# Performance work log

Hardware: AMD Instinct MI355X
Metric: run time of the kernel (lower is better)

Reference implementation:

```python
import jax, jax.numpy as jnp
import numpy as np

N_NODES = 100000
N_EDGES = 1000000
IN_DIM = 128
OUT_DIM = 64
NEG_SLOPE = 0.2


def setup_inputs() -> dict:
    key = jax.random.key(0)
    k = jax.random.split(key, 6)
    h = jax.random.normal(k[0], (N_NODES, IN_DIM), dtype=jnp.float32)
    # xavier-uniform-ish scales for linear weights
    W_w = jax.random.uniform(k[1], (OUT_DIM, IN_DIM), dtype=jnp.float32,
                             minval=-1.0, maxval=1.0) * np.sqrt(6.0 / (IN_DIM + OUT_DIM))
    W_b = jnp.zeros((OUT_DIM,), dtype=jnp.float32)
    a_w = jax.random.uniform(k[2], (1, 2 * OUT_DIM), dtype=jnp.float32,
                             minval=-1.0, maxval=1.0) * np.sqrt(6.0 / (2 * OUT_DIM + 1))
    a_b = jnp.zeros((1,), dtype=jnp.float32)
    edge_index = jax.random.randint(k[3], (2, N_EDGES), 0, N_NODES, dtype=jnp.int64)
    return {"h": h, "W_w": W_w, "W_b": W_b, "a_w": a_w, "a_b": a_b,
            "edge_index": edge_index}


def reference(h, W_w, W_b, a_w, a_b, edge_index):
    # Wh = W(h): [N, D_out]
    Wh = h @ W_w.T + W_b
    src, tgt = edge_index[0], edge_index[1]
    D = Wh.shape[1]
    # a([e_src, e_tgt]) decomposes: score = Wh@a_src per-node + Wh@a_tgt per-node,
    # gathered by edge (avoids materializing the [E, 2D] concat).
    s_src = Wh @ a_w[0, :D]   # [N]
    s_tgt = Wh @ a_w[0, D:]   # [N]
    logits = jax.nn.leaky_relu(s_src[src] + s_tgt[tgt] + a_b[0], NEG_SLOPE)  # [E]
    # NOTE: global softmax over all edges (dim=0), faithful to the source.
    attn = jax.nn.softmax(logits, axis=0)
    e_src = Wh[src]  # [E, D] gather
    messages = jnp.zeros_like(Wh).at[tgt].add(attn[:, None] * e_src)  # scatter-add
    return jax.nn.leaky_relu(messages, NEG_SLOPE)
```

## Files before the change

### kernel.cpp

```cpp
#include <hip/hip_runtime.h>
#include <math.h>

#define N_NODES 100000
#define N_EDGES 1000000
#define IN_DIM  128
#define OUT_DIM 64
#define NEG     0.2f

#define SCAN_BLOCKS 391
#define EDGE_BLOCKS 3907
#define GEMM_BLOCKS 782
#define FUSED_BLOCKS (GEMM_BLOCKS + EDGE_BLOCKS)

typedef __attribute__((ext_vector_type(8))) short short8;
typedef __attribute__((ext_vector_type(4))) float f32x4;

#define MFMA(A, B, C) __builtin_amdgcn_mfma_f32_16x16x32_bf16(A, B, C, 0, 0, 0)

union U16 { unsigned u[4]; short8 s; };

__device__ __forceinline__ void split8(const float* x, short8& hi, short8& lo) {
    U16 H, L;
#pragma unroll
    for (int i = 0; i < 4; ++i) {
        float a = x[2 * i], b = x[2 * i + 1];
        unsigned ua = __float_as_uint(a), ub = __float_as_uint(b);
        unsigned ha = ua & 0xffff0000u, hb = ub & 0xffff0000u;
        H.u[i] = (ua >> 16) | hb;
        float la = a - __uint_as_float(ha);
        float lb = b - __uint_as_float(hb);
        L.u[i] = (__float_as_uint(la) >> 16) | (__float_as_uint(lb) & 0xffff0000u);
    }
    hi = H.s; lo = L.s;
}

__global__ __launch_bounds__(256, 4) void kA_fused(
    const float* __restrict__ h, const float* __restrict__ W,
    const float* __restrict__ Wb, const float* __restrict__ aw,
    float* __restrict__ Wh, float* __restrict__ s_src, float* __restrict__ s_tgt,
    const int* __restrict__ ei, unsigned* __restrict__ deg8,
    unsigned* __restrict__ rank)
{
    __shared__ float4 smem4[2176];

    if ((blockIdx.x % 6) != 0) {
        const int hid = blockIdx.x - blockIdx.x / 6 - 1;
        const int e = hid * 256 + threadIdx.x;
        if (e < N_EDGES) {
            int t = ei[N_EDGES + e];
            rank[e] = atomicAdd(&deg8[(size_t)(hid & 7) * N_NODES + t], 1u);
        }
        return;
    }

    unsigned short* wfh = (unsigned short*)smem4;
    unsigned short* wfl = wfh + 8192;

    const int tid  = threadIdx.x;
    const int lane = tid & 63, w = tid >> 6;
    const int c = lane & 15, g = lane >> 4;
    const int n0 = (blockIdx.x / 6) * 128;

#pragma unroll
    for (int it = 0; it < 4; ++it) {
        int U = tid + 256 * it;
        int pos = U >> 6, l = U & 63;
        int nb = pos >> 2, ks = pos & 3;
        int r  = 16 * nb + (l & 15);
        int k0 = 32 * ks + 8 * (l >> 4);
        float a[8];
        *(float4*)&a[0] = *(const float4*)(W + r * IN_DIM + k0);
        *(float4*)&a[4] = *(const float4*)(W + r * IN_DIM + k0 + 4);
        short8 hi, lo; split8(a, hi, lo);
        *(short8*)(wfh + (size_t)U * 8) = hi;
        *(short8*)(wfl + (size_t)U * 8) = lo;
    }
    __syncthreads();

    const int na0 = n0 + 32 * w + c;
    const float* hp0 = h + (size_t)min(na0, N_NODES - 1) * IN_DIM + 8 * g;
    const float* hp1 = h + (size_t)min(na0 + 16, N_NODES - 1) * IN_DIM + 8 * g;

    f32x4 acc[2][4];
    {
        f32x4 z = {0.f, 0.f, 0.f, 0.f};
#pragma unroll
        for (int m = 0; m < 2; ++m)
#pragma unroll
            for (int nb = 0; nb < 4; ++nb) acc[m][nb] = z;
    }

#pragma unroll 2
    for (int ks = 0; ks < 4; ++ks) {
        short8 bh[4], bl[4];
#pragma unroll
        for (int nb = 0; nb < 4; ++nb) {
            int u = ((nb * 4 + ks) * 64 + lane) * 8;
            bh[nb] = *(const short8*)(wfh + u);
            bl[nb] = *(const short8*)(wfl + u);
        }
        float am[8];
        short8 ah, al;
        *(float4*)&am[0] = *(const float4*)(hp0 + 32 * ks);
        *(float4*)&am[4] = *(const float4*)(hp0 + 32 * ks + 4);
        split8(am, ah, al);
#pragma unroll
        for (int nb = 0; nb < 4; ++nb) {
            acc[0][nb] = MFMA(ah, bh[nb], acc[0][nb]);
            acc[0][nb] = MFMA(ah, bl[nb], acc[0][nb]);
            acc[0][nb] = MFMA(al, bh[nb], acc[0][nb]);
        }
        *(float4*)&am[0] = *(const float4*)(hp1 + 32 * ks);
        *(float4*)&am[4] = *(const float4*)(hp1 + 32 * ks + 4);
        split8(am, ah, al);
#pragma unroll
        for (int nb = 0; nb < 4; ++nb) {
            acc[1][nb] = MFMA(ah, bh[nb], acc[1][nb]);
            acc[1][nb] = MFMA(ah, bl[nb], acc[1][nb]);
            acc[1][nb] = MFMA(al, bh[nb], acc[1][nb]);
        }
    }

    float wb[4], w1[4], w2[4];
#pragma unroll
    for (int nb = 0; nb < 4; ++nb) {
        wb[nb] = Wb[16 * nb + c];
        w1[nb] = aw[16 * nb + c];
        w2[nb] = aw[OUT_DIM + 16 * nb + c];
    }
#pragma unroll
    for (int m = 0; m < 2; ++m)
#pragma unroll
        for (int r = 0; r < 4; ++r) {
            float s1 = 0.f, s2 = 0.f;
#pragma unroll
            for (int nb = 0; nb < 4; ++nb) {
                float v = acc[m][nb][r] + wb[nb];
                acc[m][nb][r] = v;
                s1 = fmaf(v, w1[nb], s1);
                s2 = fmaf(v, w2[nb], s2);
            }
#pragma unroll
            for (int mk = 1; mk < 16; mk <<= 1) {
                s1 += __shfl_xor(s1, mk);
                s2 += __shfl_xor(s2, mk);
            }
            if (c == 0) {
                int node = n0 + 32 * w + 16 * m + 4 * g + r;
                if (node < N_NODES) { s_src[node] = s1; s_tgt[node] = s2; }
            }
        }

    __syncthreads();
    float* tr = (float*)smem4;
#pragma unroll
    for (int m = 0; m < 2; ++m)
#pragma unroll
        for (int nb = 0; nb < 4; ++nb)
#pragma unroll
            for (int r = 0; r < 4; ++r)
                tr[(32 * w + 16 * m + 4 * g + r) * 68 + 16 * nb + c] = acc[m][nb][r];
    __syncthreads();

#pragma unroll
    for (int j = 0; j < 8; ++j) {
        int idx = tid + 256 * j;
        int nloc = idx >> 4, d4 = idx & 15;
        int node = n0 + nloc;
        if (node < N_NODES)
            ((float4*)Wh)[(size_t)node * 16 + d4] =
                *(const float4*)&tr[nloc * 68 + d4 * 4];
    }
}

__global__ __launch_bounds__(256) void k_mid(
    const int* __restrict__ ei, const float* __restrict__ s_src,
    const float* __restrict__ s_tgt, const float* __restrict__ ab,
    const unsigned* __restrict__ deg8,
    float* __restrict__ exv, float* __restrict__ bsum,
    unsigned* __restrict__ psum)
{
    const float ab0 = ab[0];
    float lsum = 0.f;
    const int e = blockIdx.x * 256 + threadIdx.x;
    if (e < N_EDGES) {
        int s = ei[e], t = ei[N_EDGES + e];
        float x = s_src[s] + s_tgt[t] + ab0;
        float l = x > 0.f ? x : NEG * x;
        float ex = __expf(l);
        exv[e] = ex;
        lsum = ex;
    }
#pragma unroll
    for (int off = 32; off; off >>= 1) lsum += __shfl_xor(lsum, off);
    __shared__ float ssum[4];
    if ((threadIdx.x & 63) == 0) ssum[threadIdx.x >> 6] = lsum;
    __syncthreads();
    if (threadIdx.x == 0)
        bsum[blockIdx.x] = ssum[0] + ssum[1] + ssum[2] + ssum[3];

    if (blockIdx.x < SCAN_BLOCKS) {
        const int i = blockIdx.x * 256 + threadIdx.x;
        unsigned v = 0;
        if (i < N_NODES) {
#pragma unroll
            for (int x = 0; x < 8; ++x) v += deg8[(size_t)x * N_NODES + i];
        }
#pragma unroll
        for (int off = 32; off; off >>= 1) v += __shfl_xor(v, off);
        __shared__ unsigned us[4];
        if ((threadIdx.x & 63) == 0) us[threadIdx.x >> 6] = v;
        __syncthreads();
        if (threadIdx.x == 0)
            psum[blockIdx.x] = us[0] + us[1] + us[2] + us[3];
    }
}

__global__ __launch_bounds__(512) void k_scan2(
    const unsigned* __restrict__ psum, unsigned* __restrict__ poff,
    const float* __restrict__ bsum, float* __restrict__ gsum)
{
    __shared__ unsigned sc[512];
    __shared__ float    sf[8];
    const int t = threadIdx.x;

    unsigned v = (t < SCAN_BLOCKS) ? psum[t] : 0u;
    sc[t] = v;
    __syncthreads();
    for (int off = 1; off < 512; off <<= 1) {
        unsigned u = (t >= off) ? sc[t - off] : 0u;
        __syncthreads();
        sc[t] += u;
        __syncthreads();
    }
    if (t < SCAN_BLOCKS) poff[t] = sc[t] - v;

    float s = 0.f;
    for (int i = t; i < EDGE_BLOCKS; i += 512) s += bsum[i];
#pragma unroll
    for (int off = 32; off; off >>= 1) s += __shfl_xor(s, off);
    if ((t & 63) == 0) sf[t >> 6] = s;
    __syncthreads();
    if (t == 0) {
        float tot = 0.f;
#pragma unroll
        for (int i = 0; i < 8; ++i) tot += sf[i];
        gsum[0] = tot;
    }
}

__global__ __launch_bounds__(256) void k_scan3(
    const unsigned* __restrict__ deg8, const unsigned* __restrict__ poff,
    unsigned* __restrict__ row, unsigned* __restrict__ row8)
{
    __shared__ unsigned sc[256];
    const int t = threadIdx.x;
    const int i = blockIdx.x * 256 + t;
    unsigned d[8];
    unsigned tot = 0;
    if (i < N_NODES) {
#pragma unroll
        for (int x = 0; x < 8; ++x) {
            d[x] = deg8[(size_t)x * N_NODES + i];
            tot += d[x];
        }
    }
    sc[t] = tot;
    __syncthreads();
    for (int off = 1; off < 256; off <<= 1) {
        unsigned u = (t >= off) ? sc[t - off] : 0u;
        __syncthreads();
        sc[t] += u;
        __syncthreads();
    }
    if (i < N_NODES) {
        unsigned base = poff[blockIdx.x] + sc[t] - tot;
        row[i] = base;
        unsigned run = base;
#pragma unroll
        for (int x = 0; x < 8; ++x) {
            row8[(size_t)x * N_NODES + i] = run;
            run += d[x];
        }
    }
    if (i == 0) row[N_NODES] = N_EDGES;
}

__global__ __launch_bounds__(256) void k3_fill(
    const int* __restrict__ ei, const float* __restrict__ exv,
    const unsigned* __restrict__ rank, const unsigned* __restrict__ row8,
    int2* __restrict__ bin)
{
    const int e = blockIdx.x * blockDim.x + threadIdx.x;
    if (e >= N_EDGES) return;
    int t = ei[N_EDGES + e];
    int c = (e >> 8) & 7;
    unsigned pos = row8[(size_t)c * N_NODES + t] + rank[e];
    bin[pos] = make_int2(ei[e], __float_as_int(exv[e]));
}

__global__ __launch_bounds__(256) void k_gather(
    const unsigned* __restrict__ row, const int2* __restrict__ bin,
    const float* __restrict__ gsum, const float* __restrict__ Wh,
    float* __restrict__ out)
{
    const int lane = threadIdx.x & 63;
    const int t = blockIdx.x * 4 + (threadIdx.x >> 6);
    if (t >= N_NODES) return;
    const unsigned beg = row[t], end = row[t + 1];
    float a0 = 0.f, a1 = 0.f, a2 = 0.f, a3 = 0.f;
    for (unsigned base = beg; base < end; base += 64) {
        const int cnt = (int)min(64u, end - base);
        int2 p = make_int2(0, 0);
        if (lane < cnt) p = bin[base + lane];
        int j = 0;
        for (; j + 4 <= cnt; j += 4) {
            int   s0 = __shfl(p.x, j);     float w0 = __int_as_float(__shfl(p.y, j));
            int   s1 = __shfl(p.x, j + 1); float w1 = __int_as_float(__shfl(p.y, j + 1));
            int   s2 = __shfl(p.x, j + 2); float w2 = __int_as_float(__shfl(p.y, j + 2));
            int   s3 = __shfl(p.x, j + 3); float w3 = __int_as_float(__shfl(p.y, j + 3));
            float v0 = Wh[(size_t)s0 * OUT_DIM + lane];
            float v1 = Wh[(size_t)s1 * OUT_DIM + lane];
            float v2 = Wh[(size_t)s2 * OUT_DIM + lane];
            float v3 = Wh[(size_t)s3 * OUT_DIM + lane];
            a0 = fmaf(w0, v0, a0);
            a1 = fmaf(w1, v1, a1);
            a2 = fmaf(w2, v2, a2);
            a3 = fmaf(w3, v3, a3);
        }
        for (; j < cnt; ++j) {
            int   s = __shfl(p.x, j);
            float w = __int_as_float(__shfl(p.y, j));
            a0 = fmaf(w, Wh[(size_t)s * OUT_DIM + lane], a0);
        }
    }
    float v = ((a0 + a1) + (a2 + a3)) * (1.0f / gsum[0]);
    out[(size_t)t * OUT_DIM + lane] = v > 0.f ? v : NEG * v;
}

extern "C" void kernel_launch(void* const* d_in, const int* in_sizes, int n_in,
                              void* d_out, int out_size, void* d_ws, size_t ws_size,
                              hipStream_t stream)
{
    const float* h  = (const float*)d_in[0];
    const float* W  = (const float*)d_in[1];
    const float* Wb = (const float*)d_in[2];
    const float* aw = (const float*)d_in[3];
    const float* ab = (const float*)d_in[4];
    const int*   ei = (const int*)d_in[5];

    float* ws      = (float*)d_ws;
    float* Wh      = ws;
    float* s_src   = Wh + (size_t)N_NODES * OUT_DIM;
    float* s_tgt   = s_src + N_NODES;
    unsigned* deg8   = (unsigned*)(s_tgt + N_NODES);
    unsigned* row    = deg8 + (size_t)8 * N_NODES;
    unsigned* row8   = row + N_NODES + 1;
    unsigned* psum   = row8 + (size_t)8 * N_NODES;
    unsigned* poff   = psum + 512;
    int2*     bin    = (int2*)(poff + 512);
    float*    exv    = (float*)(bin + N_EDGES);
    unsigned* rank   = (unsigned*)(exv + N_EDGES);
    float*    bsum   = (float*)(rank + N_EDGES);
    float*    gsum   = bsum + 4096;

    float* out = (float*)d_out;

    hipMemsetAsync((void*)deg8, 0, (size_t)8 * N_NODES * sizeof(unsigned), stream);

    kA_fused<<<FUSED_BLOCKS, 256, 0, stream>>>(h, W, Wb, aw, Wh, s_src, s_tgt,
                                               ei, deg8, rank);
    k_mid<<<EDGE_BLOCKS, 256, 0, stream>>>(ei, s_src, s_tgt, ab, deg8,
                                           exv, bsum, psum);
    k_scan2<<<1, 512, 0, stream>>>(psum, poff, bsum, gsum);
    k_scan3<<<SCAN_BLOCKS, 256, 0, stream>>>(deg8, poff, row, row8);
    k3_fill<<<EDGE_BLOCKS, 256, 0, stream>>>(ei, exv, rank, row8, bin);
    k_gather<<<(N_NODES + 3) / 4, 256, 0, stream>>>(row, bin, gsum, Wh, out);
}
```

Baseline: 228.7 us.

## Replace global-atomic degree histogram with LDS-chunked per-group histogram kernel

Moves the per-edge degree counting and rank assignment out of the fused GEMM kernel into a separate kernel. That kernel uses shared-memory atomics over 25000-node chunks across 32 edge groups, which also removes the memset. The aim is to replace contended global atomics with cheap LDS atomics. In exchange, each block reads its whole edge group 4 times, the per-group degree arrays grow from 8 to 32 copies (more scan traffic), and the overlap of GEMM with histogramming is lost.

```diff
diff --git a/kernel.cpp b/kernel.cpp
--- a/kernel.cpp
+++ b/kernel.cpp
@@ -9,8 +9,11 @@
 
 #define SCAN_BLOCKS 391
 #define EDGE_BLOCKS 3907
-#define GEMM_BLOCKS 782
-#define FUSED_BLOCKS (GEMM_BLOCKS + EDGE_BLOCKS)
+
+#define G_GROUPS 32
+#define EPG      (N_EDGES / G_GROUPS)
+#define CHUNK_N  25000
+#define HIST_BLOCKS (G_GROUPS * 4)
 
 typedef __attribute__((ext_vector_type(8))) short short8;
 typedef __attribute__((ext_vector_type(4))) float f32x4;
@@ -34,32 +37,19 @@
     hi = H.s; lo = L.s;
 }
 
-__global__ __launch_bounds__(256, 4) void kA_fused(
+__global__ __launch_bounds__(256, 3) void k1_mfma(
     const float* __restrict__ h, const float* __restrict__ W,
     const float* __restrict__ Wb, const float* __restrict__ aw,
-    float* __restrict__ Wh, float* __restrict__ s_src, float* __restrict__ s_tgt,
-    const int* __restrict__ ei, unsigned* __restrict__ deg8,
-    unsigned* __restrict__ rank)
+    float* __restrict__ Wh, float* __restrict__ s_src, float* __restrict__ s_tgt)
 {
     __shared__ float4 smem4[2176];
-
-    if ((blockIdx.x % 6) != 0) {
-        const int hid = blockIdx.x - blockIdx.x / 6 - 1;
-        const int e = hid * 256 + threadIdx.x;
-        if (e < N_EDGES) {
-            int t = ei[N_EDGES + e];
-            rank[e] = atomicAdd(&deg8[(size_t)(hid & 7) * N_NODES + t], 1u);
-        }
-        return;
-    }
-
     unsigned short* wfh = (unsigned short*)smem4;
     unsigned short* wfl = wfh + 8192;
 
     const int tid  = threadIdx.x;
     const int lane = tid & 63, w = tid >> 6;
     const int c = lane & 15, g = lane >> 4;
-    const int n0 = (blockIdx.x / 6) * 128;
+    const int n0 = blockIdx.x * 128;
 
 #pragma unroll
     for (int it = 0; it < 4; ++it) {
@@ -173,10 +163,38 @@
     }
 }
 
+__global__ __launch_bounds__(256) void k_hist(
+    const int* __restrict__ ei, unsigned* __restrict__ deg_g,
+    unsigned* __restrict__ rank)
+{
+    __shared__ unsigned cnt[CHUNK_N];
+    const int g  = blockIdx.x >> 2;
+    const int c0 = (blockIdx.x & 3) * CHUNK_N;
+    const int tid = threadIdx.x;
+
+    for (int i = tid; i < CHUNK_N; i += 256) cnt[i] = 0u;
+    __syncthreads();
+
+    const int ebase = g * EPG;
+    const int2* tp2 = (const int2*)(ei + N_EDGES + ebase);
+#pragma unroll 4
+    for (int i = tid; i < EPG / 2; i += 256) {
+        int2 tv = tp2[i];
+        int e0 = ebase + 2 * i;
+        unsigned u0 = (unsigned)(tv.x - c0), u1 = (unsigned)(tv.y - c0);
+        if (u0 < CHUNK_N) rank[e0]     = atomicAdd(&cnt[u0], 1u);
+        if (u1 < CHUNK_N) rank[e0 + 1] = atomicAdd(&cnt[u1], 1u);
+    }
+    __syncthreads();
+
+    unsigned* dg = deg_g + (size_t)g * N_NODES + c0;
+    for (int i = tid; i < CHUNK_N; i += 256) dg[i] = cnt[i];
+}
+
 __global__ __launch_bounds__(256) void k_mid(
     const int* __restrict__ ei, const float* __restrict__ s_src,
     const float* __restrict__ s_tgt, const float* __restrict__ ab,
-    const unsigned* __restrict__ deg8,
+    const unsigned* __restrict__ deg_g,
     float* __restrict__ exv, float* __restrict__ bsum,
     unsigned* __restrict__ psum)
 {
@@ -204,7 +222,8 @@
         unsigned v = 0;
         if (i < N_NODES) {
 #pragma unroll
-            for (int x = 0; x < 8; ++x) v += deg8[(size_t)x * N_NODES + i];
+            for (int x = 0; x < G_GROUPS; ++x)
+                v += deg_g[(size_t)x * N_NODES + i];
         }
 #pragma unroll
         for (int off = 32; off; off >>= 1) v += __shfl_xor(v, off);
@@ -250,18 +269,18 @@
 }
 
 __global__ __launch_bounds__(256) void k_scan3(
-    const unsigned* __restrict__ deg8, const unsigned* __restrict__ poff,
-    unsigned* __restrict__ row, unsigned* __restrict__ row8)
+    const unsigned* __restrict__ deg_g, const unsigned* __restrict__ poff,
+    unsigned* __restrict__ row, unsigned* __restrict__ row_g)
 {
     __shared__ unsigned sc[256];
     const int t = threadIdx.x;
     const int i = blockIdx.x * 256 + t;
-    unsigned d[8];
+    unsigned d[G_GROUPS];
     unsigned tot = 0;
     if (i < N_NODES) {
 #pragma unroll
-        for (int x = 0; x < 8; ++x) {
-            d[x] = deg8[(size_t)x * N_NODES + i];
+        for (int x = 0; x < G_GROUPS; ++x) {
+            d[x] = deg_g[(size_t)x * N_NODES + i];
             tot += d[x];
         }
     }
@@ -278,8 +297,8 @@
         row[i] = base;
         unsigned run = base;
 #pragma unroll
-        for (int x = 0; x < 8; ++x) {
-            row8[(size_t)x * N_NODES + i] = run;
+        for (int x = 0; x < G_GROUPS; ++x) {
+            row_g[(size_t)x * N_NODES + i] = run;
             run += d[x];
         }
     }
@@ -288,14 +307,14 @@
 
 __global__ __launch_bounds__(256) void k3_fill(
     const int* __restrict__ ei, const float* __restrict__ exv,
-    const unsigned* __restrict__ rank, const unsigned* __restrict__ row8,
+    const unsigned* __restrict__ rank, const unsigned* __restrict__ row_g,
     int2* __restrict__ bin)
 {
     const int e = blockIdx.x * blockDim.x + threadIdx.x;
     if (e >= N_EDGES) return;
     int t = ei[N_EDGES + e];
-    int c = (e >> 8) & 7;
-    unsigned pos = row8[(size_t)c * N_NODES + t] + rank[e];
+    int g = e / EPG;
+    unsigned pos = row_g[(size_t)g * N_NODES + t] + rank[e];
     bin[pos] = make_int2(ei[e], __float_as_int(exv[e]));
 }
 
@@ -353,10 +372,10 @@
     float* Wh      = ws;
     float* s_src   = Wh + (size_t)N_NODES * OUT_DIM;
     float* s_tgt   = s_src + N_NODES;
-    unsigned* deg8   = (unsigned*)(s_tgt + N_NODES);
-    unsigned* row    = deg8 + (size_t)8 * N_NODES;
-    unsigned* row8   = row + N_NODES + 1;
-    unsigned* psum   = row8 + (size_t)8 * N_NODES;
+    unsigned* deg_g  = (unsigned*)(s_tgt + N_NODES);
+    unsigned* row    = deg_g + (size_t)G_GROUPS * N_NODES;
+    unsigned* row_g  = row + N_NODES + 1;
+    unsigned* psum   = row_g + (size_t)G_GROUPS * N_NODES;
     unsigned* poff   = psum + 512;
     int2*     bin    = (int2*)(poff + 512);
     float*    exv    = (float*)(bin + N_EDGES);
@@ -366,14 +385,13 @@
 
     float* out = (float*)d_out;
 
-    hipMemsetAsync((void*)deg8, 0, (size_t)8 * N_NODES * sizeof(unsigned), stream);
-
-    kA_fused<<<FUSED_BLOCKS, 256, 0, stream>>>(h, W, Wb, aw, Wh, s_src, s_tgt,
-                                               ei, deg8, rank);
-    k_mid<<<EDGE_BLOCKS, 256, 0, stream>>>(ei, s_src, s_tgt, ab, deg8,
+    k_hist<<<HIST_BLOCKS, 256, 0, stream>>>(ei, deg_g, rank);
+    k1_mfma<<<(N_NODES + 127) / 128, 256, 0, stream>>>(h, W, Wb, aw, Wh,
+                                                       s_src, s_tgt);
+    k_mid<<<EDGE_BLOCKS, 256, 0, stream>>>(ei, s_src, s_tgt, ab, deg_g,
                                            exv, bsum, psum);
     k_scan2<<<1, 512, 0, stream>>>(psum, poff, bsum, gsum);
-    k_scan3<<<SCAN_BLOCKS, 256, 0, stream>>>(deg8, poff, row, row8);
-    k3_fill<<<EDGE_BLOCKS, 256, 0, stream>>>(ei, exv, rank, row8, bin);
+    k_scan3<<<SCAN_BLOCKS, 256, 0, stream>>>(deg_g, poff, row, row_g);
+    k3_fill<<<EDGE_BLOCKS, 256, 0, stream>>>(ei, exv, rank, row_g, bin);
     k_gather<<<(N_NODES + 3) / 4, 256, 0, stream>>>(row, bin, gsum, Wh, out);
 }
```

Result: no change. 231.3 us (+1.2%).
